# Performance work log

Hardware: AMD Instinct MI355X
Metric: run time of the kernel (lower is better)

Reference implementation:

```python
import jax, jax.numpy as jnp
import numpy as np

SCALES = (1, 3, 6)
PRECISION = 10  # pywt default: 2**10 samples of psi on [-5, 5]


def _gaus1_filters():
    """Replicates pywt.cwt's integrated-wavelet filters for wavelet='gaus1'.

    pywt: psi, x = wavelet.wavefun(10); int_psi = cumsum(psi)*step; per scale a:
    j = arange(a*(x[-1]-x[0])+1)/(a*step) -> int indices; filter = int_psi[j][::-1];
    conv = np.convolve(data, filter). np.convolve flips its kernel, so the
    equivalent cross-correlation kernel (lax.conv semantics) is int_psi[j].
    """
    x = np.linspace(-5.0, 5.0, 2 ** PRECISION)
    step = x[1] - x[0]
    psi = -2.0 * x * np.exp(-x ** 2) / (np.pi / 2.0) ** 0.25
    int_psi = np.cumsum(psi) * step
    filts = []
    for a in SCALES:
        j = (np.arange(a * (x[-1] - x[0]) + 1) / (a * step)).astype(np.int64)
        j = j[j < int_psi.size]
        filts.append(int_psi[j].astype(np.float32))  # correlation kernel
    return filts

_FILTS = _gaus1_filters()


def setup_inputs() -> dict:
    key = jax.random.key(0)
    x = jax.random.normal(key, (32, 4096, 64), dtype=jnp.float32)
    return {"x": x}


def reference(x):
    B, S, C = x.shape
    sig = jnp.transpose(x, (0, 2, 1)).reshape(B * C, 1, S)  # [B*C, 1, S]
    outs = []
    for a, f in zip(SCALES, _FILTS):
        L = f.shape[0]
        k = jnp.asarray(f).reshape(1, 1, L)
        # full convolution (np.convolve): pad L-1 both sides
        conv = jax.lax.conv_general_dilated(
            sig, k, window_strides=(1,), padding=[(L - 1, L - 1)],
            dimension_numbers=("NCH", "OIH", "NCH"))  # [B*C, 1, S+L-1]
        coef = -np.sqrt(a).astype(np.float32) * jnp.diff(conv, axis=-1)  # [B*C,1,S+L-2]
        d = (coef.shape[-1] - S) / 2.0
        coef = coef[..., int(np.floor(d)): coef.shape[-1] - int(np.ceil(d))]  # [B*C,1,S]
        outs.append(coef)
    out = jnp.concatenate(outs, axis=1).reshape(B, C, len(SCALES), S)
    return jnp.transpose(out, (0, 2, 3, 1))  # [B, 3, S, C]
```

## Files before the change

kernel.cpp:

```cpp
#include <hip/hip_runtime.h>
#include <math.h>

#define S_LEN  4096
#define NCH    64
#define TILE_S 64
#define RPT    8
#define TY     8
#define HALO_L 31
#define STAGE  (TILE_S + 61)
#define WLEN   (61 + RPT)
#define PRE    12

struct WtArgs { float w6[62]; float w3[32]; float w1[12]; };


template <int T, int R>
struct FmaR {
  static __device__ __forceinline__ void run(const WtArgs& W, const float (&win)[WLEN],
                                             float (&a6)[RPT], float (&a3)[RPT],
                                             float (&a1)[RPT]) {
    a6[R] = fmaf(W.w6[T], win[T + R], a6[R]);
    if constexpr (T >= 15 && T <= 46) a3[R] = fmaf(W.w3[T - 15], win[T + R], a3[R]);
    if constexpr (T >= 25 && T <= 36) a1[R] = fmaf(W.w1[T - 25], win[T + R], a1[R]);
    FmaR<T, R + 1>::run(W, win, a6, a3, a1);
  }
};
template <int T>
struct FmaR<T, RPT> {
  static __device__ __forceinline__ void run(const WtArgs&, const float (&)[WLEN],
                                             float (&)[RPT], float (&)[RPT], float (&)[RPT]) {}
};

template <int T>
struct Step {
  static __device__ __forceinline__ void run(const float* __restrict__ col, const WtArgs& W,
                                             float (&win)[WLEN], float (&a6)[RPT],
                                             float (&a3)[RPT], float (&a1)[RPT]) {
    if constexpr (T + PRE < WLEN) win[T + PRE] = col[(T + PRE) * NCH];
    FmaR<T, 0>::run(W, win, a6, a3, a1);
    Step<T + 1>::run(col, W, win, a6, a3, a1);
  }
};
template <>
struct Step<62> {
  static __device__ __forceinline__ void run(const float* __restrict__, const WtArgs&,
                                             float (&)[WLEN], float (&)[RPT],
                                             float (&)[RPT], float (&)[RPT]) {}
};

template <int K>
struct Pre {
  static __device__ __forceinline__ void run(const float* __restrict__ col, float (&win)[WLEN]) {
    win[K] = col[K * NCH];
    Pre<K + 1>::run(col, win);
  }
};
template <>
struct Pre<PRE> {
  static __device__ __forceinline__ void run(const float* __restrict__, float (&)[WLEN]) {}
};

template <int R>
struct Store {
  static __device__ __forceinline__ void run(float* __restrict__ o1, float* __restrict__ o3,
                                             float* __restrict__ o6, const float (&a6)[RPT],
                                             const float (&a3)[RPT], const float (&a1)[RPT]) {
    o1[(size_t)R * NCH] = a1[R];
    o3[(size_t)R * NCH] = a3[R];
    o6[(size_t)R * NCH] = a6[R];
    Store<R + 1>::run(o1, o3, o6, a6, a3, a1);
  }
};
template <>
struct Store<RPT> {
  static __device__ __forceinline__ void run(float* __restrict__, float* __restrict__,
                                             float* __restrict__, const float (&)[RPT],
                                             const float (&)[RPT], const float (&)[RPT]) {}
};

template <int R>
struct Zero {
  static __device__ __forceinline__ void run(float (&a6)[RPT], float (&a3)[RPT], float (&a1)[RPT]) {
    a6[R] = 0.f; a3[R] = 0.f; a1[R] = 0.f;
    Zero<R + 1>::run(a6, a3, a1);
  }
};
template <>
struct Zero<RPT> {
  static __device__ __forceinline__ void run(float (&)[RPT], float (&)[RPT], float (&)[RPT]) {}
};

__global__ __launch_bounds__(512, 8)
void cwt_main(const float* __restrict__ x, float* __restrict__ out, const WtArgs W) {
  __shared__ __align__(16) float lds[STAGE * NCH];

  const int c   = threadIdx.x;
  const int ty  = threadIdx.y;
  const int tid = ty * 64 + c;

  const int hw  = blockIdx.x;
  const int wg  = ((hw & 7) << 8) + (hw >> 3);
  const int sx  = wg & 63;
  const int b   = wg >> 6;
  const int s0  = sx * TILE_S;

  const float* xb = x + (size_t)b * S_LEN * NCH;
  const int row0 = s0 - HALO_L;

  float4 stg[4];
  #pragma unroll
  for (int i = 0; i < 4; ++i) {
    const int idx = tid + i * 512;
    const int r = idx >> 4, q = idx & 15;
    const int row = row0 + r;
    float4 v = make_float4(0.f, 0.f, 0.f, 0.f);
    if (idx < STAGE * 16 && row >= 0 && row < S_LEN)
      v = *(const float4*)(xb + ((size_t)row * NCH + (q << 2)));
    stg[i] = v;
  }
  #pragma unroll
  for (int i = 0; i < 4; ++i) {
    const int idx = tid + i * 512;
    if (idx < STAGE * 16)
      *(float4*)(&lds[(idx >> 4) * NCH + ((idx & 15) << 2)]) = stg[i];
  }
  __syncthreads();

  const int base = ty * RPT;
  const float* col = &lds[base * NCH + c];

  float win[WLEN];
  float a6[RPT], a3[RPT], a1[RPT];
  Zero<0>::run(a6, a3, a1);
  Pre<0>::run(col, win);
  Step<0>::run(col, W, win, a6, a3, a1);

  const int srow = s0 + base;
  float* o1 = out + (((size_t)b * 3 + 0) * S_LEN + srow) * NCH + c;
  float* o3 = out + (((size_t)b * 3 + 1) * S_LEN + srow) * NCH + c;
  float* o6 = out + (((size_t)b * 3 + 2) * S_LEN + srow) * NCH + c;
  Store<0>::run(o1, o3, o6, a6, a3, a1);
}

extern "C" void kernel_launch(void* const* d_in, const int* in_sizes, int n_in,
                              void* d_out, int out_size, void* d_ws, size_t ws_size,
                              hipStream_t stream) {
  (void)n_in; (void)out_size; (void)d_ws; (void)ws_size;
  const float* x = (const float*)d_in[0];
  float* out = (float*)d_out;
  const int B = in_sizes[0] / (S_LEN * NCH);

  WtArgs W;
  {
    static double ip[1024];
    const double delta = 10.0 / 1023.0;
    const double step  = (-5.0 + delta) + 5.0;
    const double cn    = pow(3.141592653589793 * 0.5, 0.25);
    double s = 0.0;
    for (int i = 0; i < 1024; ++i) {
      const double xi  = (i == 1023) ? 5.0 : ((double)i * delta - 5.0);
      const double psi = (-2.0 * xi) * exp(-(xi * xi)) / cn;
      s += psi;
      ip[i] = s * step;
    }
    const int   as_[3] = {6, 3, 1};
    const int   lf_[3] = {61, 31, 11};
    float*      wp_[3] = {W.w6, W.w3, W.w1};
    for (int si = 0; si < 3; ++si) {
      const double denom = (double)as_[si] * step;
      const float  sqa   = (float)sqrt((double)as_[si]);
      const int    lf    = lf_[si];
      for (int t = 0; t <= lf; ++t) {
        float km1 = 0.f, kt = 0.f;
        if (t >= 1)      km1 = (float)ip[(long)(((double)(t - 1)) / denom)];
        if (t <= lf - 1) kt  = (float)ip[(long)(((double)t) / denom)];
        wp_[si][t] = -sqa * (km1 - kt);
      }
    }
  }

  const int nblk = (S_LEN / TILE_S) * B;
  dim3 grid(nblk);
  dim3 block(NCH, TY);
  hipLaunchKernelGGL(cwt_main, grid, block, 0, stream, x, out, W);
}
```

Baseline: 137.4 us.

## Read input directly from global memory instead of staging through LDS

Removes the shared-memory staging tile and its barrier. Each thread now loads its 69-row sliding window straight from global memory, relying on the cache to serve the heavily overlapping rows between threads. Boundary tiles get a separate bounds-checked instantiation, and the prefetch depth is raised from 12 to 20 with launch bounds lowered to 6 waves. The risk is much more redundant global/L2 traffic, about 8.6x re-reads per element, plus higher register pressure from the deeper prefetch.

```diff
diff --git a/kernel.cpp b/kernel.cpp
--- a/kernel.cpp
+++ b/kernel.cpp
@@ -7,9 +7,8 @@
 #define RPT    8
 #define TY     8
 #define HALO_L 31
-#define STAGE  (TILE_S + 61)
 #define WLEN   (61 + RPT)
-#define PRE    12
+#define PRE    20
 
 struct WtArgs { float w6[62]; float w3[32]; float w1[12]; };
 
@@ -31,33 +30,49 @@
                                              float (&)[RPT], float (&)[RPT], float (&)[RPT]) {}
 };
 
-template <int T>
-struct Step {
-  static __device__ __forceinline__ void run(const float* __restrict__ col, const WtArgs& W,
-                                             float (&win)[WLEN], float (&a6)[RPT],
-                                             float (&a3)[RPT], float (&a1)[RPT]) {
-    if constexpr (T + PRE < WLEN) win[T + PRE] = col[(T + PRE) * NCH];
-    FmaR<T, 0>::run(W, win, a6, a3, a1);
-    Step<T + 1>::run(col, W, win, a6, a3, a1);
+template <int K, bool G>
+struct Pre {
+  static __device__ __forceinline__ void run(const float* __restrict__ col, int rowbase,
+                                             float (&win)[WLEN]) {
+    if constexpr (G) {
+      float v = 0.f;
+      if ((unsigned)(rowbase + K) < (unsigned)S_LEN) v = col[K * NCH];
+      win[K] = v;
+    } else {
+      win[K] = col[K * NCH];
+    }
+    Pre<K + 1, G>::run(col, rowbase, win);
   }
 };
-template <>
-struct Step<62> {
-  static __device__ __forceinline__ void run(const float* __restrict__, const WtArgs&,
+template <bool G>
+struct Pre<PRE, G> {
+  static __device__ __forceinline__ void run(const float* __restrict__, int, float (&)[WLEN]) {}
+};
+
+template <int T, bool G>
+struct Step {
+  static __device__ __forceinline__ void run(const float* __restrict__ col, int rowbase,
+                                             const WtArgs& W, float (&win)[WLEN],
+                                             float (&a6)[RPT], float (&a3)[RPT],
+                                             float (&a1)[RPT]) {
+    if constexpr (T + PRE < WLEN) {
+      if constexpr (G) {
+        float v = 0.f;
+        if ((unsigned)(rowbase + T + PRE) < (unsigned)S_LEN) v = col[(T + PRE) * NCH];
+        win[T + PRE] = v;
+      } else {
+        win[T + PRE] = col[(T + PRE) * NCH];
+      }
+    }
+    FmaR<T, 0>::run(W, win, a6, a3, a1);
+    Step<T + 1, G>::run(col, rowbase, W, win, a6, a3, a1);
+  }
+};
+template <bool G>
+struct Step<62, G> {
+  static __device__ __forceinline__ void run(const float* __restrict__, int, const WtArgs&,
                                              float (&)[WLEN], float (&)[RPT],
                                              float (&)[RPT], float (&)[RPT]) {}
-};
-
-template <int K>
-struct Pre {
-  static __device__ __forceinline__ void run(const float* __restrict__ col, float (&win)[WLEN]) {
-    win[K] = col[K * NCH];
-    Pre<K + 1>::run(col, win);
-  }
-};
-template <>
-struct Pre<PRE> {
-  static __device__ __forceinline__ void run(const float* __restrict__, float (&)[WLEN]) {}
 };
 
 template <int R>
@@ -90,13 +105,10 @@
   static __device__ __forceinline__ void run(float (&)[RPT], float (&)[RPT], float (&)[RPT]) {}
 };
 
-__global__ __launch_bounds__(512, 8)
+__global__ __launch_bounds__(512, 6)
 void cwt_main(const float* __restrict__ x, float* __restrict__ out, const WtArgs W) {
-  __shared__ __align__(16) float lds[STAGE * NCH];
-
   const int c   = threadIdx.x;
   const int ty  = threadIdx.y;
-  const int tid = ty * 64 + c;
 
   const int hw  = blockIdx.x;
   const int wg  = ((hw & 7) << 8) + (hw >> 3);
@@ -105,37 +117,22 @@
   const int s0  = sx * TILE_S;
 
   const float* xb = x + (size_t)b * S_LEN * NCH;
-  const int row0 = s0 - HALO_L;
-
-  float4 stg[4];
-  #pragma unroll
-  for (int i = 0; i < 4; ++i) {
-    const int idx = tid + i * 512;
-    const int r = idx >> 4, q = idx & 15;
-    const int row = row0 + r;
-    float4 v = make_float4(0.f, 0.f, 0.f, 0.f);
-    if (idx < STAGE * 16 && row >= 0 && row < S_LEN)
-      v = *(const float4*)(xb + ((size_t)row * NCH + (q << 2)));
-    stg[i] = v;
-  }
-  #pragma unroll
-  for (int i = 0; i < 4; ++i) {
-    const int idx = tid + i * 512;
-    if (idx < STAGE * 16)
-      *(float4*)(&lds[(idx >> 4) * NCH + ((idx & 15) << 2)]) = stg[i];
-  }
-  __syncthreads();
-
-  const int base = ty * RPT;
-  const float* col = &lds[base * NCH + c];
+  const int rowbase = s0 - HALO_L + ty * RPT;
+  const float* col  = xb + (ptrdiff_t)rowbase * NCH + c;
 
   float win[WLEN];
   float a6[RPT], a3[RPT], a1[RPT];
   Zero<0>::run(a6, a3, a1);
-  Pre<0>::run(col, win);
-  Step<0>::run(col, W, win, a6, a3, a1);
 
-  const int srow = s0 + base;
+  if (sx >= 1 && sx <= 62) {
+    Pre<0, false>::run(col, rowbase, win);
+    Step<0, false>::run(col, rowbase, W, win, a6, a3, a1);
+  } else {
+    Pre<0, true>::run(col, rowbase, win);
+    Step<0, true>::run(col, rowbase, W, win, a6, a3, a1);
+  }
+
+  const int srow = s0 + ty * RPT;
   float* o1 = out + (((size_t)b * 3 + 0) * S_LEN + srow) * NCH + c;
   float* o3 = out + (((size_t)b * 3 + 1) * S_LEN + srow) * NCH + c;
   float* o6 = out + (((size_t)b * 3 + 2) * S_LEN + srow) * NCH + c;
```

Result: slower. 165.2 us (+20.2%).
